# Performance work log

Hardware: AMD Instinct MI355X
Metric: run time of the kernel (lower is better)

Reference implementation:

```python
import jax, jax.numpy as jnp
import numpy as np

# dims / hyperparams (mirror init_kwargs)
B, N, C, K = 256, 16000, 32, 64          # batch, samples, cochlear channels, gammatone taps
FS, FMIN, FMAX, BWF = 16000, 100.0, 8000.0, 1.0
WINDOW, STRIDE = 256, 128                # inner hair cell framing -> T = 124
ANS, HID, OUT = 10, 50, 10               # auditory-nerve fanout, bushy/ic hidden, AC out
BETA, THR = 0.95, 1.0                    # snn.Leaky(beta=0.95), threshold 1.0, subtract reset
AN_LO, AN_HI, AN_THR = 0.5, 1.5, 0.5     # an_range scales + AN firing threshold

# Heaviside spike with ATan surrogate gradient (snntorch default style)
@jax.custom_vjp
def spike(u):
    return (u > 0).astype(u.dtype)

def _spike_fwd(u):
    return spike(u), u

def _spike_bwd(u, g):
    return (g / (1.0 + (jnp.pi * u) ** 2),)

spike.defvjp(_spike_fwd, _spike_bwd)

def _gammatone_bank():
    # ERB-spaced 4th-order gammatone impulse responses, unit L2 norm. [C, K]
    def hz2erb(f):
        return 21.4 * np.log10(1.0 + 0.00437 * f)
    def erb2hz(e):
        return (10.0 ** (e / 21.4) - 1.0) / 0.00437
    cfs = erb2hz(np.linspace(hz2erb(FMIN), hz2erb(FMAX), C))
    b = BWF * 1.019 * 24.7 * (4.37 * cfs / 1000.0 + 1.0)
    t = np.arange(K) / FS
    ker = (t[None, :] ** 3) * np.exp(-2 * np.pi * b[:, None] * t[None, :]) \
          * np.cos(2 * np.pi * cfs[:, None] * t[None, :])
    ker = ker / (np.linalg.norm(ker, axis=1, keepdims=True) + 1e-12)
    return jnp.asarray(ker, jnp.float32)

def setup_inputs() -> dict:
    key = jax.random.key(0)
    k1, k2, k3, k4 = jax.random.split(key, 4)
    audio = jax.random.normal(k1, (B, N), dtype=jnp.float32)
    W_bushy = jax.random.normal(k2, (HID, C * ANS), dtype=jnp.float32) / np.sqrt(C * ANS)
    W_ic = jax.random.normal(k3, (HID, HID), dtype=jnp.float32) / np.sqrt(HID)
    W_ac = jax.random.normal(k4, (OUT, HID), dtype=jnp.float32) / np.sqrt(HID)
    return {"audio": audio, "gt_kernels": _gammatone_bank(),
            "W_bushy": W_bushy, "W_ic": W_ic, "W_ac": W_ac}

def reference(audio, gt_kernels, W_bushy, W_ic, W_ac):
    # Cochlear: gammatone filterbank, [B,1,N] conv [C,1,K] SAME -> [B,C,N]
    y = jax.lax.conv_general_dilated(audio[:, None, :], gt_kernels[:, None, :],
                                     window_strides=(1,), padding="SAME")
    # InnerHairCell: half-wave rectify + moving-average framing -> [B,C,T]
    y = jnp.maximum(y, 0.0)
    env = jax.lax.reduce_window(y, 0.0, jax.lax.add,
                                (1, 1, WINDOW), (1, 1, STRIDE), "VALID") / WINDOW
    frames = jnp.transpose(env, (2, 0, 1))  # [T,B,C]
    scales = jnp.linspace(AN_LO, AN_HI, ANS, dtype=jnp.float32)

    def lif(mem, cur):
        mem = BETA * mem + cur
        spk = spike(mem - THR)
        return spk, mem - THR * spk  # subtract reset

    def step(carry, x_t):  # x_t [B,C]
        mem_b, mem_ic, mem_ac = carry
        # AuditoryNerve: ans scaled copies per channel, threshold fire -> [B, C*ANS]
        spk_an = spike(x_t[:, :, None] * scales - AN_THR).reshape(x_t.shape[0], -1)
        spk_b, mem_b = lif(mem_b, spk_an @ W_bushy.T)     # Bushy
        spk_ic, mem_ic = lif(mem_ic, spk_b @ W_ic.T)      # InferiorColliculus
        spk_ac, mem_ac = lif(mem_ac, spk_ic @ W_ac.T)     # AudioCortex
        return (mem_b, mem_ic, mem_ac), (spk_ac, mem_ac)

    bsz = audio.shape[0]
    init = (jnp.zeros((bsz, HID), audio.dtype),
            jnp.zeros((bsz, HID), audio.dtype),
            jnp.zeros((bsz, OUT), audio.dtype))
    _, (spk_rec, mem_rec) = jax.lax.scan(step, init, frames)
    # stack along dim=1 as in torch code -> [B,T,OUT]
    return jnp.transpose(spk_rec, (1, 0, 2)), jnp.transpose(mem_rec, (1, 0, 2))
```

## Files before the change

### kernel.cpp

```cpp
#include <hip/hip_runtime.h>

#define B_   256
#define N_   16000
#define C_   32
#define K_   64
#define T_   124
#define NJ   125
#define HID_ 50
#define OUT_ 10
#define TB_  1024
#define CURS 52

typedef unsigned int u32;
typedef float v2f __attribute__((ext_vector_type(2)));
struct __align__(16) f2x2 { v2f lo, hi; };

__device__ __forceinline__ float fadd(float a, float b) { return __fadd_rn(a, b); }
__device__ __forceinline__ float fmul(float a, float b) { return __fmul_rn(a, b); }
__device__ __forceinline__ float fsub(float a, float b) { return __fsub_rn(a, b); }

__device__ __forceinline__ void PKFMA(v2f& y, v2f a, const f2x2& T, int k) {
    switch (k) {
    case 0:  asm("v_pk_fma_f32 %0, %1, %2, %0 op_sel:[0,0,0] op_sel_hi:[1,0,1]"
                 : "+v"(y) : "v"(a), "s"(T.lo)); break;
    case 1:  asm("v_pk_fma_f32 %0, %1, %2, %0 op_sel:[0,1,0] op_sel_hi:[1,1,1]"
                 : "+v"(y) : "v"(a), "s"(T.lo)); break;
    case 2:  asm("v_pk_fma_f32 %0, %1, %2, %0 op_sel:[0,0,0] op_sel_hi:[1,0,1]"
                 : "+v"(y) : "v"(a), "s"(T.hi)); break;
    default: asm("v_pk_fma_f32 %0, %1, %2, %0 op_sel:[0,1,0] op_sel_hi:[1,1,1]"
                 : "+v"(y) : "v"(a), "s"(T.hi)); break;
    }
}

__global__ __launch_bounds__(256, 4) void convA(const float* __restrict__ audio,
                                                const float* __restrict__ gt,
                                                float* __restrict__ Sg) {
    __shared__ __align__(16) float abI[1280];
    __shared__ __align__(16) float ybuf[4][4][272];

    const int b = blockIdx.x, g = blockIdx.y;
    const int tid = threadIdx.x, w = tid >> 6, lane = tid & 63;
    const float* arow = audio + (size_t)b * N_;

    const int origin = (g << 10) - 32;
    for (int idx = tid; idx < 1280; idx += 256) {
        int P = idx / 640, j = idx - P * 640;
        int ii = j >> 1, h = j & 1;
        int gi = origin + (P << 9) + (h << 8) + ii;
        float v = (gi >= 0 && gi < N_) ? arow[gi] : 0.0f;
        abI[P * 640 + (j ^ (((j >> 5) & 1) << 2))] = v;
    }
    __syncthreads();

    for (int G = 0; G < 2; ++G) {
        const int rowbase = __builtin_amdgcn_readfirstlane(((w << 3) + (G << 2)) << 6);
        const float* kg = gt + rowbase;

        v2f Y[2][4][4];
#pragma unroll
        for (int P = 0; P < 2; ++P)
#pragma unroll
            for (int ch = 0; ch < 4; ++ch)
#pragma unroll
                for (int d = 0; d < 4; ++d) { Y[P][ch][d].x = 0.0f; Y[P][ch][d].y = 0.0f; }

        {
            f2x2 Tc[4];
#pragma unroll
            for (int ch = 0; ch < 4; ++ch)
                Tc[ch] = *(const f2x2*)(kg + (ch << 6));
            const int u = lane;
            const int p1 = (u << 3) ^ (((u >> 2) & 1) << 2);
#pragma unroll
            for (int P = 0; P < 2; ++P) {
                const float* abP = abI + P * 640;
                const f2x2 A0 = *(const f2x2*)(abP + p1);
                const f2x2 A1 = *(const f2x2*)(abP + (p1 ^ 4));
#pragma unroll
                for (int e = 0; e < 4; ++e) {
                    const v2f a = (e == 0) ? A0.lo : (e == 1) ? A0.hi
                                : (e == 2) ? A1.lo : A1.hi;
#pragma unroll
                    for (int ch = 0; ch < 4; ++ch)
#pragma unroll
                        for (int d = 0; d < 4; ++d) {
                            const int kb = e - 1 - d;
                            if (kb >= 0) PKFMA(Y[P][ch][d], a, Tc[ch], kb);
                        }
                }
            }
        }

#pragma unroll 1
        for (int q = 1; q < 16; ++q) {
            f2x2 Tm[4], Tc[4];
#pragma unroll
            for (int ch = 0; ch < 4; ++ch) {
                Tm[ch] = *(const f2x2*)(kg + (ch << 6) + ((q - 1) << 2));
                Tc[ch] = *(const f2x2*)(kg + (ch << 6) + (q << 2));
            }
            const int u = lane + q;
            const int p1 = (u << 3) ^ (((u >> 2) & 1) << 2);
#pragma unroll
            for (int P = 0; P < 2; ++P) {
                const float* abP = abI + P * 640;
                const f2x2 A0 = *(const f2x2*)(abP + p1);
                const f2x2 A1 = *(const f2x2*)(abP + (p1 ^ 4));
#pragma unroll
                for (int e = 0; e < 4; ++e) {
                    const v2f a = (e == 0) ? A0.lo : (e == 1) ? A0.hi
                                : (e == 2) ? A1.lo : A1.hi;
#pragma unroll
                    for (int ch = 0; ch < 4; ++ch)
#pragma unroll
                        for (int d = 0; d < 4; ++d) {
                            const int ts = e - 1 - d;
                            if (ts >= 0) PKFMA(Y[P][ch][d], a, Tc[ch], ts);
                            else         PKFMA(Y[P][ch][d], a, Tm[ch], 4 + ts);
                        }
                }
            }
        }

        {
            f2x2 Tm[4];
#pragma unroll
            for (int ch = 0; ch < 4; ++ch)
                Tm[ch] = *(const f2x2*)(kg + (ch << 6) + 60);
            const int u = lane + 16;
            const int p1 = (u << 3) ^ (((u >> 2) & 1) << 2);
#pragma unroll
            for (int P = 0; P < 2; ++P) {
                const float* abP = abI + P * 640;
                const f2x2 A0 = *(const f2x2*)(abP + p1);
                const f2x2 A1 = *(const f2x2*)(abP + (p1 ^ 4));
#pragma unroll
                for (int e = 0; e < 4; ++e) {
                    const v2f a = (e == 0) ? A0.lo : (e == 1) ? A0.hi
                                : (e == 2) ? A1.lo : A1.hi;
#pragma unroll
                    for (int ch = 0; ch < 4; ++ch)
#pragma unroll
                        for (int d = 0; d < 4; ++d) {
                            const int ts = e - 1 - d;
                            if (ts < 0) PKFMA(Y[P][ch][d], a, Tm[ch], 4 + ts);
                        }
                }
            }
        }

#pragma unroll
        for (int pp = 0; pp < 4; ++pp) {
            const int P = pp >> 1, h = pp & 1;
#pragma unroll
            for (int ch = 0; ch < 4; ++ch) {
                float4 z;
                z.x = fmaxf(h ? Y[P][ch][0].y : Y[P][ch][0].x, 0.0f);
                z.y = fmaxf(h ? Y[P][ch][1].y : Y[P][ch][1].x, 0.0f);
                z.z = fmaxf(h ? Y[P][ch][2].y : Y[P][ch][2].x, 0.0f);
                z.w = fmaxf(h ? Y[P][ch][3].y : Y[P][ch][3].x, 0.0f);
                *(float4*)(&ybuf[w][ch][((lane >> 5) * 136) + ((lane & 31) << 2)]) = z;
            }
            {
                const int ch2 = lane >> 4, blk = (lane >> 3) & 1, j = lane & 7;
                const float* yb = &ybuf[w][ch2][blk * 136 + j];
                float r = yb[0];
#pragma unroll
                for (int m = 1; m < 16; ++m) r = fadd(r, yb[m << 3]);
                float v = fadd(r, __shfl_xor(r, 1));
                v = fadd(v, __shfl_xor(v, 2));
                v = fadd(v, __shfl_xor(v, 4));
                const int jg = (g << 3) + (pp << 1) + blk;
                const int c = (w << 3) + (G << 2) + ch2;
                if (j == 0 && jg < NJ) Sg[((size_t)b * C_ + c) * NJ + jg] = v;
            }
        }
    }
}

__global__ __launch_bounds__(TB_, 1) void snnB(const float* __restrict__ Sg,
                                               const float* __restrict__ Wb,
                                               const float* __restrict__ Wic,
                                               const float* __restrict__ Wac,
                                               float* __restrict__ out) {
    __shared__ float sWb[HID_ * 321];
    __shared__ __align__(16) float sWic[HID_ * 52];
    __shared__ __align__(16) float sWac[OUT_ * 52];
    __shared__ u32   mask[128 * 10];
    __shared__ __align__(16) float cur[T_ * CURS];
    __shared__ __align__(16) float icur[T_ * CURS];
    __shared__ float acur[T_ * 12];

    const int b = blockIdx.x, tid = threadIdx.x;

    for (int i = tid; i < HID_ * 320; i += TB_) {
        int r = i / 320;
        sWb[r * 321 + (i - r * 320)] = Wb[i];
    }
    for (int i = tid; i < HID_ * HID_; i += TB_) {
        int r = i / 50;
        sWic[r * 52 + (i - r * 50)] = Wic[i];
    }
    for (int i = tid; i < OUT_ * HID_; i += TB_) {
        int r = i / 50;
        sWac[r * 52 + (i - r * 50)] = Wac[i];
    }

    const float* Sb = Sg + (size_t)b * C_ * NJ;
    for (int idx = tid; idx < 1280; idx += TB_) {
        if (idx >= T_ * 10) { mask[idx] = 0; continue; }
        int t = idx / 10, wd = idx - t * 10;
        u32 m = 0;
        int c_prev = -1;
        float env = 0.0f;
        for (int k = 0; k < 32; ++k) {
            int i = wd * 32 + k;
            int c = i / 10, s = i - c * 10;
            if (c != c_prev) {
                env = fmul(fadd(Sb[c * NJ + t], Sb[c * NJ + t + 1]), 0.00390625f);
                c_prev = c;
            }
            float sf = (s == 9) ? 1.5f : (float)(0.5 + (double)s * (1.0 / 9.0));
            if (fsub(fmul(env, sf), 0.5f) > 0.0f) m |= (1u << k);
        }
        mask[idx] = m;
    }
    __syncthreads();

    if (tid < 16 * HID_) {
        const int t0 = tid / 50, h = tid - t0 * 50;
        const float* wr = sWb + h * 321;
        const u32* mrow = mask + t0 * 10;
        float a0 = 0.0f, a1 = 0.0f, a2 = 0.0f, a3 = 0.0f;
        float a4 = 0.0f, a5 = 0.0f, a6 = 0.0f, a7 = 0.0f;
#pragma unroll 1
        for (int wi = 0; wi < 10; ++wi) {
            const u32 w0 = mrow[wi], w1 = mrow[160 + wi];
            const u32 w2 = mrow[320 + wi], w3 = mrow[480 + wi];
            const u32 w4 = mrow[640 + wi], w5 = mrow[800 + wi];
            const u32 w6 = mrow[960 + wi], w7 = mrow[1120 + wi];
#pragma unroll
            for (int b2 = 0; b2 < 32; ++b2) {
                const float wv = wr[(wi << 5) + b2];
                const int iw = __float_as_int(wv);
                a0 = fadd(a0, __int_as_float(iw & __builtin_amdgcn_sbfe((int)w0, b2, 1)));
                a1 = fadd(a1, __int_as_float(iw & __builtin_amdgcn_sbfe((int)w1, b2, 1)));
                a2 = fadd(a2, __int_as_float(iw & __builtin_amdgcn_sbfe((int)w2, b2, 1)));
                a3 = fadd(a3, __int_as_float(iw & __builtin_amdgcn_sbfe((int)w3, b2, 1)));
                a4 = fadd(a4, __int_as_float(iw & __builtin_amdgcn_sbfe((int)w4, b2, 1)));
                a5 = fadd(a5, __int_as_float(iw & __builtin_amdgcn_sbfe((int)w5, b2, 1)));
                a6 = fadd(a6, __int_as_float(iw & __builtin_amdgcn_sbfe((int)w6, b2, 1)));
                a7 = fadd(a7, __int_as_float(iw & __builtin_amdgcn_sbfe((int)w7, b2, 1)));
            }
        }
        cur[(t0      ) * CURS + h] = a0;
        cur[(t0 + 16 ) * CURS + h] = a1;
        cur[(t0 + 32 ) * CURS + h] = a2;
        cur[(t0 + 48 ) * CURS + h] = a3;
        cur[(t0 + 64 ) * CURS + h] = a4;
        cur[(t0 + 80 ) * CURS + h] = a5;
        cur[(t0 + 96 ) * CURS + h] = a6;
        if (t0 + 112 < T_) cur[(t0 + 112) * CURS + h] = a7;
    }
    __syncthreads();

    if (tid < HID_) {
        float mem = 0.0f;
        for (int t0 = 0; t0 < 120; t0 += 8) {
            float c0[8];
#pragma unroll
            for (int k = 0; k < 8; ++k) c0[k] = cur[(t0 + k) * CURS + tid];
#pragma unroll
            for (int k = 0; k < 8; ++k) {
                float m = fadd(fmul(0.95f, mem), c0[k]);
                float sp = (fsub(m, 1.0f) > 0.0f) ? 1.0f : 0.0f;
                mem = fsub(m, sp);
                cur[(t0 + k) * CURS + tid] = sp;
            }
        }
        for (int t = 120; t < T_; ++t) {
            float m = fadd(fmul(0.95f, mem), cur[t * CURS + tid]);
            float sp = (fsub(m, 1.0f) > 0.0f) ? 1.0f : 0.0f;
            mem = fsub(m, sp);
            cur[t * CURS + tid] = sp;
        }
    }
    __syncthreads();

    for (int idx = tid; idx < T_ * 25; idx += TB_) {
        int t = idx / 25, hp = idx - t * 25;
        const float* w0 = sWic + hp * 52;
        const float* w1 = sWic + (hp + 25) * 52;
        const float* sb = cur + t * CURS;
        float acc0 = 0.0f, acc1 = 0.0f;
#pragma unroll
        for (int g4 = 0; g4 < 12; ++g4) {
            const float4 s4 = *(const float4*)(sb + (g4 << 2));
            const float4 wa = *(const float4*)(w0 + (g4 << 2));
            const float4 wb = *(const float4*)(w1 + (g4 << 2));
            acc0 = fmaf(s4.x, wa.x, acc0);  acc1 = fmaf(s4.x, wb.x, acc1);
            acc0 = fmaf(s4.y, wa.y, acc0);  acc1 = fmaf(s4.y, wb.y, acc1);
            acc0 = fmaf(s4.z, wa.z, acc0);  acc1 = fmaf(s4.z, wb.z, acc1);
            acc0 = fmaf(s4.w, wa.w, acc0);  acc1 = fmaf(s4.w, wb.w, acc1);
        }
        acc0 = fmaf(sb[48], w0[48], acc0);  acc1 = fmaf(sb[48], w1[48], acc1);
        acc0 = fmaf(sb[49], w0[49], acc0);  acc1 = fmaf(sb[49], w1[49], acc1);
        icur[t * CURS + hp] = acc0;
        icur[t * CURS + hp + 25] = acc1;
    }
    __syncthreads();

    if (tid < HID_) {
        float mem = 0.0f;
        for (int t0 = 0; t0 < 120; t0 += 8) {
            float c0[8];
#pragma unroll
            for (int k = 0; k < 8; ++k) c0[k] = icur[(t0 + k) * CURS + tid];
#pragma unroll
            for (int k = 0; k < 8; ++k) {
                float m = fadd(fmul(0.95f, mem), c0[k]);
                float sp = (fsub(m, 1.0f) > 0.0f) ? 1.0f : 0.0f;
                mem = fsub(m, sp);
                icur[(t0 + k) * CURS + tid] = sp;
            }
        }
        for (int t = 120; t < T_; ++t) {
            float m = fadd(fmul(0.95f, mem), icur[t * CURS + tid]);
            float sp = (fsub(m, 1.0f) > 0.0f) ? 1.0f : 0.0f;
            mem = fsub(m, sp);
            icur[t * CURS + tid] = sp;
        }
    }
    __syncthreads();

    for (int idx = tid; idx < T_ * 5; idx += TB_) {
        int t = idx / 5, op = idx - t * 5;
        const float* w0 = sWac + op * 52;
        const float* w1 = sWac + (op + 5) * 52;
        const float* sb = icur + t * CURS;
        float acc0 = 0.0f, acc1 = 0.0f;
#pragma unroll
        for (int g4 = 0; g4 < 12; ++g4) {
            const float4 s4 = *(const float4*)(sb + (g4 << 2));
            const float4 wa = *(const float4*)(w0 + (g4 << 2));
            const float4 wb = *(const float4*)(w1 + (g4 << 2));
            acc0 = fmaf(s4.x, wa.x, acc0);  acc1 = fmaf(s4.x, wb.x, acc1);
            acc0 = fmaf(s4.y, wa.y, acc0);  acc1 = fmaf(s4.y, wb.y, acc1);
            acc0 = fmaf(s4.z, wa.z, acc0);  acc1 = fmaf(s4.z, wb.z, acc1);
            acc0 = fmaf(s4.w, wa.w, acc0);  acc1 = fmaf(s4.w, wb.w, acc1);
        }
        acc0 = fmaf(sb[48], w0[48], acc0);  acc1 = fmaf(sb[48], w1[48], acc1);
        acc0 = fmaf(sb[49], w0[49], acc0);  acc1 = fmaf(sb[49], w1[49], acc1);
        acur[t * 12 + op] = acc0;
        acur[t * 12 + op + 5] = acc1;
    }
    __syncthreads();

    if (tid < OUT_) {
        float mem = 0.0f;
        for (int t0 = 0; t0 < 120; t0 += 8) {
            float c0[8];
#pragma unroll
            for (int k = 0; k < 8; ++k) c0[k] = acur[(t0 + k) * 12 + tid];
#pragma unroll
            for (int k = 0; k < 8; ++k) {
                float m = fadd(fmul(0.95f, mem), c0[k]);
                float sp = (fsub(m, 1.0f) > 0.0f) ? 1.0f : 0.0f;
                float mo = fsub(m, sp);
                mem = mo;
                size_t base = ((size_t)b * T_ + (t0 + k)) * OUT_ + tid;
                out[base] = sp;
                out[(size_t)(B_ * T_ * OUT_) + base] = mo;
            }
        }
        for (int t = 120; t < T_; ++t) {
            float m = fadd(fmul(0.95f, mem), acur[t * 12 + tid]);
            float sp = (fsub(m, 1.0f) > 0.0f) ? 1.0f : 0.0f;
            float mo = fsub(m, sp);
            mem = mo;
            size_t base = ((size_t)b * T_ + t) * OUT_ + tid;
            out[base] = sp;
            out[(size_t)(B_ * T_ * OUT_) + base] = mo;
        }
    }
}

extern "C" void kernel_launch(void* const* d_in, const int* in_sizes, int n_in,
                              void* d_out, int out_size, void* d_ws, size_t ws_size,
                              hipStream_t stream) {
    (void)in_sizes; (void)n_in; (void)out_size; (void)ws_size;
    const float* audio = (const float*)d_in[0];
    const float* gt    = (const float*)d_in[1];
    const float* Wb    = (const float*)d_in[2];
    const float* Wic   = (const float*)d_in[3];
    const float* Wac   = (const float*)d_in[4];

    float* Sg = (float*)d_ws;

    convA<<<dim3(B_, 16), dim3(256), 0, stream>>>(audio, gt, Sg);
    snnB<<<dim3(B_), dim3(TB_), 0, stream>>>(Sg, Wb, Wic, Wac, (float*)d_out);
}
```

Before: 309.1 us.

## Split conv accumulators per half-block to raise occupancy; pack SNN adds

The conv kernel's loop is reordered so the P (audio half) loop is outermost with a single 4x4 accumulator set instead of 2x4x4, and launch bounds move from 4 to 6 waves per SIMD. The aim is to lower register pressure and raise occupancy. The cost is that the kernel taps are reloaded once per P. Separately, the bushy-current accumulation packs pairs of accumulators into v2f vectors so the compiler can emit packed f32 adds.

New measurement: 308.4 us. Within noise of the previous version (-0.2%).

```diff
diff --git a/kernel.cpp b/kernel.cpp
--- a/kernel.cpp
+++ b/kernel.cpp
@@ -32,7 +32,7 @@
     }
 }
 
-__global__ __launch_bounds__(256, 4) void convA(const float* __restrict__ audio,
+__global__ __launch_bounds__(256, 6) void convA(const float* __restrict__ audio,
                                                 const float* __restrict__ gt,
                                                 float* __restrict__ Sg) {
     __shared__ __align__(16) float abI[1280];
@@ -52,28 +52,27 @@
     }
     __syncthreads();
 
-    for (int G = 0; G < 2; ++G) {
-        const int rowbase = __builtin_amdgcn_readfirstlane(((w << 3) + (G << 2)) << 6);
-        const float* kg = gt + rowbase;
-
-        v2f Y[2][4][4];
-#pragma unroll
-        for (int P = 0; P < 2; ++P)
+#pragma unroll 1
+    for (int P = 0; P < 2; ++P) {
+        const float* abP = abI + P * 640;
+#pragma unroll 1
+        for (int G = 0; G < 2; ++G) {
+            const int rowbase = __builtin_amdgcn_readfirstlane(((w << 3) + (G << 2)) << 6);
+            const float* kg = gt + rowbase;
+
+            v2f Y[4][4];
 #pragma unroll
             for (int ch = 0; ch < 4; ++ch)
 #pragma unroll
-                for (int d = 0; d < 4; ++d) { Y[P][ch][d].x = 0.0f; Y[P][ch][d].y = 0.0f; }
-
-        {
-            f2x2 Tc[4];
-#pragma unroll
-            for (int ch = 0; ch < 4; ++ch)
-                Tc[ch] = *(const f2x2*)(kg + (ch << 6));
-            const int u = lane;
-            const int p1 = (u << 3) ^ (((u >> 2) & 1) << 2);
-#pragma unroll
-            for (int P = 0; P < 2; ++P) {
-                const float* abP = abI + P * 640;
+                for (int d = 0; d < 4; ++d) { Y[ch][d].x = 0.0f; Y[ch][d].y = 0.0f; }
+
+            {
+                f2x2 Tc[4];
+#pragma unroll
+                for (int ch = 0; ch < 4; ++ch)
+                    Tc[ch] = *(const f2x2*)(kg + (ch << 6));
+                const int u = lane;
+                const int p1 = (u << 3) ^ (((u >> 2) & 1) << 2);
                 const f2x2 A0 = *(const f2x2*)(abP + p1);
                 const f2x2 A1 = *(const f2x2*)(abP + (p1 ^ 4));
 #pragma unroll
@@ -85,25 +84,21 @@
 #pragma unroll
                         for (int d = 0; d < 4; ++d) {
                             const int kb = e - 1 - d;
-                            if (kb >= 0) PKFMA(Y[P][ch][d], a, Tc[ch], kb);
+                            if (kb >= 0) PKFMA(Y[ch][d], a, Tc[ch], kb);
                         }
                 }
             }
-        }
 
 #pragma unroll 1
-        for (int q = 1; q < 16; ++q) {
-            f2x2 Tm[4], Tc[4];
-#pragma unroll
-            for (int ch = 0; ch < 4; ++ch) {
-                Tm[ch] = *(const f2x2*)(kg + (ch << 6) + ((q - 1) << 2));
-                Tc[ch] = *(const f2x2*)(kg + (ch << 6) + (q << 2));
-            }
-            const int u = lane + q;
-            const int p1 = (u << 3) ^ (((u >> 2) & 1) << 2);
-#pragma unroll
-            for (int P = 0; P < 2; ++P) {
-                const float* abP = abI + P * 640;
+            for (int q = 1; q < 16; ++q) {
+                f2x2 Tm[4], Tc[4];
+#pragma unroll
+                for (int ch = 0; ch < 4; ++ch) {
+                    Tm[ch] = *(const f2x2*)(kg + (ch << 6) + ((q - 1) << 2));
+                    Tc[ch] = *(const f2x2*)(kg + (ch << 6) + (q << 2));
+                }
+                const int u = lane + q;
+                const int p1 = (u << 3) ^ (((u >> 2) & 1) << 2);
                 const f2x2 A0 = *(const f2x2*)(abP + p1);
                 const f2x2 A1 = *(const f2x2*)(abP + (p1 ^ 4));
 #pragma unroll
@@ -115,23 +110,19 @@
 #pragma unroll
                         for (int d = 0; d < 4; ++d) {
                             const int ts = e - 1 - d;
-                            if (ts >= 0) PKFMA(Y[P][ch][d], a, Tc[ch], ts);
-                            else         PKFMA(Y[P][ch][d], a, Tm[ch], 4 + ts);
+                            if (ts >= 0) PKFMA(Y[ch][d], a, Tc[ch], ts);
+                            else         PKFMA(Y[ch][d], a, Tm[ch], 4 + ts);
                         }
                 }
             }
-        }
-
-        {
-            f2x2 Tm[4];
-#pragma unroll
-            for (int ch = 0; ch < 4; ++ch)
-                Tm[ch] = *(const f2x2*)(kg + (ch << 6) + 60);
-            const int u = lane + 16;
-            const int p1 = (u << 3) ^ (((u >> 2) & 1) << 2);
-#pragma unroll
-            for (int P = 0; P < 2; ++P) {
-                const float* abP = abI + P * 640;
+
+            {
+                f2x2 Tm[4];
+#pragma unroll
+                for (int ch = 0; ch < 4; ++ch)
+                    Tm[ch] = *(const f2x2*)(kg + (ch << 6) + 60);
+                const int u = lane + 16;
+                const int p1 = (u << 3) ^ (((u >> 2) & 1) << 2);
                 const f2x2 A0 = *(const f2x2*)(abP + p1);
                 const f2x2 A1 = *(const f2x2*)(abP + (p1 ^ 4));
 #pragma unroll
@@ -143,36 +134,36 @@
 #pragma unroll
                         for (int d = 0; d < 4; ++d) {
                             const int ts = e - 1 - d;
-                            if (ts < 0) PKFMA(Y[P][ch][d], a, Tm[ch], 4 + ts);
+                            if (ts < 0) PKFMA(Y[ch][d], a, Tm[ch], 4 + ts);
                         }
                 }
             }
-        }
-
-#pragma unroll
-        for (int pp = 0; pp < 4; ++pp) {
-            const int P = pp >> 1, h = pp & 1;
-#pragma unroll
-            for (int ch = 0; ch < 4; ++ch) {
-                float4 z;
-                z.x = fmaxf(h ? Y[P][ch][0].y : Y[P][ch][0].x, 0.0f);
-                z.y = fmaxf(h ? Y[P][ch][1].y : Y[P][ch][1].x, 0.0f);
-                z.z = fmaxf(h ? Y[P][ch][2].y : Y[P][ch][2].x, 0.0f);
-                z.w = fmaxf(h ? Y[P][ch][3].y : Y[P][ch][3].x, 0.0f);
-                *(float4*)(&ybuf[w][ch][((lane >> 5) * 136) + ((lane & 31) << 2)]) = z;
-            }
-            {
-                const int ch2 = lane >> 4, blk = (lane >> 3) & 1, j = lane & 7;
-                const float* yb = &ybuf[w][ch2][blk * 136 + j];
-                float r = yb[0];
-#pragma unroll
-                for (int m = 1; m < 16; ++m) r = fadd(r, yb[m << 3]);
-                float v = fadd(r, __shfl_xor(r, 1));
-                v = fadd(v, __shfl_xor(v, 2));
-                v = fadd(v, __shfl_xor(v, 4));
-                const int jg = (g << 3) + (pp << 1) + blk;
-                const int c = (w << 3) + (G << 2) + ch2;
-                if (j == 0 && jg < NJ) Sg[((size_t)b * C_ + c) * NJ + jg] = v;
+
+#pragma unroll
+            for (int h = 0; h < 2; ++h) {
+                const int pp = (P << 1) + h;
+#pragma unroll
+                for (int ch = 0; ch < 4; ++ch) {
+                    float4 z;
+                    z.x = fmaxf(h ? Y[ch][0].y : Y[ch][0].x, 0.0f);
+                    z.y = fmaxf(h ? Y[ch][1].y : Y[ch][1].x, 0.0f);
+                    z.z = fmaxf(h ? Y[ch][2].y : Y[ch][2].x, 0.0f);
+                    z.w = fmaxf(h ? Y[ch][3].y : Y[ch][3].x, 0.0f);
+                    *(float4*)(&ybuf[w][ch][((lane >> 5) * 136) + ((lane & 31) << 2)]) = z;
+                }
+                {
+                    const int ch2 = lane >> 4, blk = (lane >> 3) & 1, j = lane & 7;
+                    const float* yb = &ybuf[w][ch2][blk * 136 + j];
+                    float r = yb[0];
+#pragma unroll
+                    for (int m = 1; m < 16; ++m) r = fadd(r, yb[m << 3]);
+                    float v = fadd(r, __shfl_xor(r, 1));
+                    v = fadd(v, __shfl_xor(v, 2));
+                    v = fadd(v, __shfl_xor(v, 4));
+                    const int jg = (g << 3) + (pp << 1) + blk;
+                    const int c = (w << 3) + (G << 2) + ch2;
+                    if (j == 0 && jg < NJ) Sg[((size_t)b * C_ + c) * NJ + jg] = v;
+                }
             }
         }
     }
@@ -231,8 +222,8 @@
         const int t0 = tid / 50, h = tid - t0 * 50;
         const float* wr = sWb + h * 321;
         const u32* mrow = mask + t0 * 10;
-        float a0 = 0.0f, a1 = 0.0f, a2 = 0.0f, a3 = 0.0f;
-        float a4 = 0.0f, a5 = 0.0f, a6 = 0.0f, a7 = 0.0f;
+        v2f A0v = {0.0f, 0.0f}, A1v = {0.0f, 0.0f};
+        v2f A2v = {0.0f, 0.0f}, A3v = {0.0f, 0.0f};
 #pragma unroll 1
         for (int wi = 0; wi < 10; ++wi) {
             const u32 w0 = mrow[wi], w1 = mrow[160 + wi];
@@ -243,24 +234,29 @@
             for (int b2 = 0; b2 < 32; ++b2) {
                 const float wv = wr[(wi << 5) + b2];
                 const int iw = __float_as_int(wv);
-                a0 = fadd(a0, __int_as_float(iw & __builtin_amdgcn_sbfe((int)w0, b2, 1)));
-                a1 = fadd(a1, __int_as_float(iw & __builtin_amdgcn_sbfe((int)w1, b2, 1)));
-                a2 = fadd(a2, __int_as_float(iw & __builtin_amdgcn_sbfe((int)w2, b2, 1)));
-                a3 = fadd(a3, __int_as_float(iw & __builtin_amdgcn_sbfe((int)w3, b2, 1)));
-                a4 = fadd(a4, __int_as_float(iw & __builtin_amdgcn_sbfe((int)w4, b2, 1)));
-                a5 = fadd(a5, __int_as_float(iw & __builtin_amdgcn_sbfe((int)w5, b2, 1)));
-                a6 = fadd(a6, __int_as_float(iw & __builtin_amdgcn_sbfe((int)w6, b2, 1)));
-                a7 = fadd(a7, __int_as_float(iw & __builtin_amdgcn_sbfe((int)w7, b2, 1)));
-            }
-        }
-        cur[(t0      ) * CURS + h] = a0;
-        cur[(t0 + 16 ) * CURS + h] = a1;
-        cur[(t0 + 32 ) * CURS + h] = a2;
-        cur[(t0 + 48 ) * CURS + h] = a3;
-        cur[(t0 + 64 ) * CURS + h] = a4;
-        cur[(t0 + 80 ) * CURS + h] = a5;
-        cur[(t0 + 96 ) * CURS + h] = a6;
-        if (t0 + 112 < T_) cur[(t0 + 112) * CURS + h] = a7;
+                v2f p0, p1, p2, p3;
+                p0.x = __int_as_float(iw & __builtin_amdgcn_sbfe((int)w0, b2, 1));
+                p0.y = __int_as_float(iw & __builtin_amdgcn_sbfe((int)w1, b2, 1));
+                p1.x = __int_as_float(iw & __builtin_amdgcn_sbfe((int)w2, b2, 1));
+                p1.y = __int_as_float(iw & __builtin_amdgcn_sbfe((int)w3, b2, 1));
+                p2.x = __int_as_float(iw & __builtin_amdgcn_sbfe((int)w4, b2, 1));
+                p2.y = __int_as_float(iw & __builtin_amdgcn_sbfe((int)w5, b2, 1));
+                p3.x = __int_as_float(iw & __builtin_amdgcn_sbfe((int)w6, b2, 1));
+                p3.y = __int_as_float(iw & __builtin_amdgcn_sbfe((int)w7, b2, 1));
+                A0v = A0v + p0;
+                A1v = A1v + p1;
+                A2v = A2v + p2;
+                A3v = A3v + p3;
+            }
+        }
+        cur[(t0      ) * CURS + h] = A0v.x;
+        cur[(t0 + 16 ) * CURS + h] = A0v.y;
+        cur[(t0 + 32 ) * CURS + h] = A1v.x;
+        cur[(t0 + 48 ) * CURS + h] = A1v.y;
+        cur[(t0 + 64 ) * CURS + h] = A2v.x;
+        cur[(t0 + 80 ) * CURS + h] = A2v.y;
+        cur[(t0 + 96 ) * CURS + h] = A3v.x;
+        if (t0 + 112 < T_) cur[(t0 + 112) * CURS + h] = A3v.y;
     }
     __syncthreads();
 
```

## Retile SNN bushy/IC/AC matmuls as 2x4 register tiles with packed adds

Applied to the files above, without the earlier changes.

The bushy-layer masked accumulation now has each thread compute two hidden units across four timesteps, with paired v2f adds, instead of one hidden unit across eight timesteps. Weight-row stride goes to 324 and the weights are loaded with float4 copies. The IC and AC projections are retiled the same way (4 timesteps x 2 outputs per thread, 775 or 155 threads) so each weight vector load is reused across timesteps. The aim is fewer LDS loads per FLOP and more ILP in the SNN kernel, at the cost of more registers per thread and changed LDS bank patterns.

Measured after the change: 290.7 us, median of 2. 6.0% less time.

```diff
diff --git a/kernel.cpp b/kernel.cpp
--- a/kernel.cpp
+++ b/kernel.cpp
@@ -10,6 +10,7 @@
 #define OUT_ 10
 #define TB_  1024
 #define CURS 52
+#define WBS  324
 
 typedef unsigned int u32;
 typedef float v2f __attribute__((ext_vector_type(2)));
@@ -183,7 +184,7 @@
                                                const float* __restrict__ Wic,
                                                const float* __restrict__ Wac,
                                                float* __restrict__ out) {
-    __shared__ float sWb[HID_ * 321];
+    __shared__ __align__(16) float sWb[HID_ * WBS];
     __shared__ __align__(16) float sWic[HID_ * 52];
     __shared__ __align__(16) float sWac[OUT_ * 52];
     __shared__ u32   mask[128 * 10];
@@ -193,9 +194,10 @@
 
     const int b = blockIdx.x, tid = threadIdx.x;
 
-    for (int i = tid; i < HID_ * 320; i += TB_) {
-        int r = i / 320;
-        sWb[r * 321 + (i - r * 320)] = Wb[i];
+    for (int i4 = tid; i4 < 4000; i4 += TB_) {
+        const int i = i4 << 2;
+        const int r = i / 320, col = i - r * 320;
+        *(float4*)(&sWb[r * WBS + col]) = *(const float4*)(Wb + i);
     }
     for (int i = tid; i < HID_ * HID_; i += TB_) {
         int r = i / 50;
@@ -227,40 +229,41 @@
     }
     __syncthreads();
 
-    if (tid < 16 * HID_) {
-        const int t0 = tid / 50, h = tid - t0 * 50;
-        const float* wr = sWb + h * 321;
+    if (tid < 31 * 25) {
+        const int t0 = tid / 25, hp = tid - t0 * 25;
+        const float* wr0 = sWb + hp * WBS;
+        const float* wr1 = sWb + (hp + 25) * WBS;
         const u32* mrow = mask + t0 * 10;
-        float a0 = 0.0f, a1 = 0.0f, a2 = 0.0f, a3 = 0.0f;
-        float a4 = 0.0f, a5 = 0.0f, a6 = 0.0f, a7 = 0.0f;
+        v2f a0 = {0.0f, 0.0f}, a1 = {0.0f, 0.0f};
+        v2f a2 = {0.0f, 0.0f}, a3 = {0.0f, 0.0f};
 #pragma unroll 1
         for (int wi = 0; wi < 10; ++wi) {
-            const u32 w0 = mrow[wi], w1 = mrow[160 + wi];
-            const u32 w2 = mrow[320 + wi], w3 = mrow[480 + wi];
-            const u32 w4 = mrow[640 + wi], w5 = mrow[800 + wi];
-            const u32 w6 = mrow[960 + wi], w7 = mrow[1120 + wi];
+            const u32 w0 = mrow[wi],       w1 = mrow[310 + wi];
+            const u32 w2 = mrow[620 + wi], w3 = mrow[930 + wi];
 #pragma unroll
             for (int b2 = 0; b2 < 32; ++b2) {
-                const float wv = wr[(wi << 5) + b2];
-                const int iw = __float_as_int(wv);
-                a0 = fadd(a0, __int_as_float(iw & __builtin_amdgcn_sbfe((int)w0, b2, 1)));
-                a1 = fadd(a1, __int_as_float(iw & __builtin_amdgcn_sbfe((int)w1, b2, 1)));
-                a2 = fadd(a2, __int_as_float(iw & __builtin_amdgcn_sbfe((int)w2, b2, 1)));
-                a3 = fadd(a3, __int_as_float(iw & __builtin_amdgcn_sbfe((int)w3, b2, 1)));
-                a4 = fadd(a4, __int_as_float(iw & __builtin_amdgcn_sbfe((int)w4, b2, 1)));
-                a5 = fadd(a5, __int_as_float(iw & __builtin_amdgcn_sbfe((int)w5, b2, 1)));
-                a6 = fadd(a6, __int_as_float(iw & __builtin_amdgcn_sbfe((int)w6, b2, 1)));
-                a7 = fadd(a7, __int_as_float(iw & __builtin_amdgcn_sbfe((int)w7, b2, 1)));
-            }
-        }
-        cur[(t0      ) * CURS + h] = a0;
-        cur[(t0 + 16 ) * CURS + h] = a1;
-        cur[(t0 + 32 ) * CURS + h] = a2;
-        cur[(t0 + 48 ) * CURS + h] = a3;
-        cur[(t0 + 64 ) * CURS + h] = a4;
-        cur[(t0 + 80 ) * CURS + h] = a5;
-        cur[(t0 + 96 ) * CURS + h] = a6;
-        if (t0 + 112 < T_) cur[(t0 + 112) * CURS + h] = a7;
+                const int i = (wi << 5) + b2;
+                const int iw0 = __float_as_int(wr0[i]);
+                const int iw1 = __float_as_int(wr1[i]);
+                const int s0 = __builtin_amdgcn_sbfe((int)w0, b2, 1);
+                const int s1 = __builtin_amdgcn_sbfe((int)w1, b2, 1);
+                const int s2 = __builtin_amdgcn_sbfe((int)w2, b2, 1);
+                const int s3 = __builtin_amdgcn_sbfe((int)w3, b2, 1);
+                v2f p0, p1, p2, p3;
+                p0.x = __int_as_float(iw0 & s0);  p0.y = __int_as_float(iw1 & s0);
+                p1.x = __int_as_float(iw0 & s1);  p1.y = __int_as_float(iw1 & s1);
+                p2.x = __int_as_float(iw0 & s2);  p2.y = __int_as_float(iw1 & s2);
+                p3.x = __int_as_float(iw0 & s3);  p3.y = __int_as_float(iw1 & s3);
+                a0 = a0 + p0;
+                a1 = a1 + p1;
+                a2 = a2 + p2;
+                a3 = a3 + p3;
+            }
+        }
+        cur[(t0     ) * CURS + hp] = a0.x;  cur[(t0     ) * CURS + hp + 25] = a0.y;
+        cur[(t0 + 31) * CURS + hp] = a1.x;  cur[(t0 + 31) * CURS + hp + 25] = a1.y;
+        cur[(t0 + 62) * CURS + hp] = a2.x;  cur[(t0 + 62) * CURS + hp + 25] = a2.y;
+        cur[(t0 + 93) * CURS + hp] = a3.x;  cur[(t0 + 93) * CURS + hp + 25] = a3.y;
     }
     __syncthreads();
 
@@ -287,26 +290,53 @@
     }
     __syncthreads();
 
-    for (int idx = tid; idx < T_ * 25; idx += TB_) {
-        int t = idx / 25, hp = idx - t * 25;
+    if (tid < 31 * 25) {
+        const int t0 = tid / 25, hp = tid - t0 * 25;
         const float* w0 = sWic + hp * 52;
         const float* w1 = sWic + (hp + 25) * 52;
-        const float* sb = cur + t * CURS;
-        float acc0 = 0.0f, acc1 = 0.0f;
+        const float* sb0 = cur + (t0     ) * CURS;
+        const float* sb1 = cur + (t0 + 31) * CURS;
+        const float* sb2 = cur + (t0 + 62) * CURS;
+        const float* sb3 = cur + (t0 + 93) * CURS;
+        float A00 = 0.0f, A01 = 0.0f, A10 = 0.0f, A11 = 0.0f;
+        float A20 = 0.0f, A21 = 0.0f, A30 = 0.0f, A31 = 0.0f;
 #pragma unroll
         for (int g4 = 0; g4 < 12; ++g4) {
-            const float4 s4 = *(const float4*)(sb + (g4 << 2));
             const float4 wa = *(const float4*)(w0 + (g4 << 2));
             const float4 wb = *(const float4*)(w1 + (g4 << 2));
-            acc0 = fmaf(s4.x, wa.x, acc0);  acc1 = fmaf(s4.x, wb.x, acc1);
-            acc0 = fmaf(s4.y, wa.y, acc0);  acc1 = fmaf(s4.y, wb.y, acc1);
-            acc0 = fmaf(s4.z, wa.z, acc0);  acc1 = fmaf(s4.z, wb.z, acc1);
-            acc0 = fmaf(s4.w, wa.w, acc0);  acc1 = fmaf(s4.w, wb.w, acc1);
-        }
-        acc0 = fmaf(sb[48], w0[48], acc0);  acc1 = fmaf(sb[48], w1[48], acc1);
-        acc0 = fmaf(sb[49], w0[49], acc0);  acc1 = fmaf(sb[49], w1[49], acc1);
-        icur[t * CURS + hp] = acc0;
-        icur[t * CURS + hp + 25] = acc1;
+            const float4 s0 = *(const float4*)(sb0 + (g4 << 2));
+            const float4 s1 = *(const float4*)(sb1 + (g4 << 2));
+            const float4 s2 = *(const float4*)(sb2 + (g4 << 2));
+            const float4 s3 = *(const float4*)(sb3 + (g4 << 2));
+            A00 = fmaf(s0.x, wa.x, A00); A00 = fmaf(s0.y, wa.y, A00);
+            A00 = fmaf(s0.z, wa.z, A00); A00 = fmaf(s0.w, wa.w, A00);
+            A01 = fmaf(s0.x, wb.x, A01); A01 = fmaf(s0.y, wb.y, A01);
+            A01 = fmaf(s0.z, wb.z, A01); A01 = fmaf(s0.w, wb.w, A01);
+            A10 = fmaf(s1.x, wa.x, A10); A10 = fmaf(s1.y, wa.y, A10);
+            A10 = fmaf(s1.z, wa.z, A10); A10 = fmaf(s1.w, wa.w, A10);
+            A11 = fmaf(s1.x, wb.x, A11); A11 = fmaf(s1.y, wb.y, A11);
+            A11 = fmaf(s1.z, wb.z, A11); A11 = fmaf(s1.w, wb.w, A11);
+            A20 = fmaf(s2.x, wa.x, A20); A20 = fmaf(s2.y, wa.y, A20);
+            A20 = fmaf(s2.z, wa.z, A20); A20 = fmaf(s2.w, wa.w, A20);
+            A21 = fmaf(s2.x, wb.x, A21); A21 = fmaf(s2.y, wb.y, A21);
+            A21 = fmaf(s2.z, wb.z, A21); A21 = fmaf(s2.w, wb.w, A21);
+            A30 = fmaf(s3.x, wa.x, A30); A30 = fmaf(s3.y, wa.y, A30);
+            A30 = fmaf(s3.z, wa.z, A30); A30 = fmaf(s3.w, wa.w, A30);
+            A31 = fmaf(s3.x, wb.x, A31); A31 = fmaf(s3.y, wb.y, A31);
+            A31 = fmaf(s3.z, wb.z, A31); A31 = fmaf(s3.w, wb.w, A31);
+        }
+        A00 = fmaf(sb0[48], w0[48], A00); A00 = fmaf(sb0[49], w0[49], A00);
+        A01 = fmaf(sb0[48], w1[48], A01); A01 = fmaf(sb0[49], w1[49], A01);
+        A10 = fmaf(sb1[48], w0[48], A10); A10 = fmaf(sb1[49], w0[49], A10);
+        A11 = fmaf(sb1[48], w1[48], A11); A11 = fmaf(sb1[49], w1[49], A11);
+        A20 = fmaf(sb2[48], w0[48], A20); A20 = fmaf(sb2[49], w0[49], A20);
+        A21 = fmaf(sb2[48], w1[48], A21); A21 = fmaf(sb2[49], w1[49], A21);
+        A30 = fmaf(sb3[48], w0[48], A30); A30 = fmaf(sb3[49], w0[49], A30);
+        A31 = fmaf(sb3[48], w1[48], A31); A31 = fmaf(sb3[49], w1[49], A31);
+        icur[(t0     ) * CURS + hp] = A00;  icur[(t0     ) * CURS + hp + 25] = A01;
+        icur[(t0 + 31) * CURS + hp] = A10;  icur[(t0 + 31) * CURS + hp + 25] = A11;
+        icur[(t0 + 62) * CURS + hp] = A20;  icur[(t0 + 62) * CURS + hp + 25] = A21;
+        icur[(t0 + 93) * CURS + hp] = A30;  icur[(t0 + 93) * CURS + hp + 25] = A31;
     }
     __syncthreads();
 
@@ -333,26 +363,53 @@
     }
     __syncthreads();
 
-    for (int idx = tid; idx < T_ * 5; idx += TB_) {
-        int t = idx / 5, op = idx - t * 5;
+    if (tid < 31 * 5) {
+        const int t0 = tid / 5, op = tid - t0 * 5;
         const float* w0 = sWac + op * 52;
         const float* w1 = sWac + (op + 5) * 52;
-        const float* sb = icur + t * CURS;
-        float acc0 = 0.0f, acc1 = 0.0f;
+        const float* sb0 = icur + (t0     ) * CURS;
+        const float* sb1 = icur + (t0 + 31) * CURS;
+        const float* sb2 = icur + (t0 + 62) * CURS;
+        const float* sb3 = icur + (t0 + 93) * CURS;
+        float A00 = 0.0f, A01 = 0.0f, A10 = 0.0f, A11 = 0.0f;
+        float A20 = 0.0f, A21 = 0.0f, A30 = 0.0f, A31 = 0.0f;
 #pragma unroll
         for (int g4 = 0; g4 < 12; ++g4) {
-            const float4 s4 = *(const float4*)(sb + (g4 << 2));
             const float4 wa = *(const float4*)(w0 + (g4 << 2));
             const float4 wb = *(const float4*)(w1 + (g4 << 2));
-            acc0 = fmaf(s4.x, wa.x, acc0);  acc1 = fmaf(s4.x, wb.x, acc1);
-            acc0 = fmaf(s4.y, wa.y, acc0);  acc1 = fmaf(s4.y, wb.y, acc1);
-            acc0 = fmaf(s4.z, wa.z, acc0);  acc1 = fmaf(s4.z, wb.z, acc1);
-            acc0 = fmaf(s4.w, wa.w, acc0);  acc1 = fmaf(s4.w, wb.w, acc1);
-        }
-        acc0 = fmaf(sb[48], w0[48], acc0);  acc1 = fmaf(sb[48], w1[48], acc1);
-        acc0 = fmaf(sb[49], w0[49], acc0);  acc1 = fmaf(sb[49], w1[49], acc1);
-        acur[t * 12 + op] = acc0;
-        acur[t * 12 + op + 5] = acc1;
+            const float4 s0 = *(const float4*)(sb0 + (g4 << 2));
+            const float4 s1 = *(const float4*)(sb1 + (g4 << 2));
+            const float4 s2 = *(const float4*)(sb2 + (g4 << 2));
+            const float4 s3 = *(const float4*)(sb3 + (g4 << 2));
+            A00 = fmaf(s0.x, wa.x, A00); A00 = fmaf(s0.y, wa.y, A00);
+            A00 = fmaf(s0.z, wa.z, A00); A00 = fmaf(s0.w, wa.w, A00);
+            A01 = fmaf(s0.x, wb.x, A01); A01 = fmaf(s0.y, wb.y, A01);
+            A01 = fmaf(s0.z, wb.z, A01); A01 = fmaf(s0.w, wb.w, A01);
+            A10 = fmaf(s1.x, wa.x, A10); A10 = fmaf(s1.y, wa.y, A10);
+            A10 = fmaf(s1.z, wa.z, A10); A10 = fmaf(s1.w, wa.w, A10);
+            A11 = fmaf(s1.x, wb.x, A11); A11 = fmaf(s1.y, wb.y, A11);
+            A11 = fmaf(s1.z, wb.z, A11); A11 = fmaf(s1.w, wb.w, A11);
+            A20 = fmaf(s2.x, wa.x, A20); A20 = fmaf(s2.y, wa.y, A20);
+            A20 = fmaf(s2.z, wa.z, A20); A20 = fmaf(s2.w, wa.w, A20);
+            A21 = fmaf(s2.x, wb.x, A21); A21 = fmaf(s2.y, wb.y, A21);
+            A21 = fmaf(s2.z, wb.z, A21); A21 = fmaf(s2.w, wb.w, A21);
+            A30 = fmaf(s3.x, wa.x, A30); A30 = fmaf(s3.y, wa.y, A30);
+            A30 = fmaf(s3.z, wa.z, A30); A30 = fmaf(s3.w, wa.w, A30);
+            A31 = fmaf(s3.x, wb.x, A31); A31 = fmaf(s3.y, wb.y, A31);
+            A31 = fmaf(s3.z, wb.z, A31); A31 = fmaf(s3.w, wb.w, A31);
+        }
+        A00 = fmaf(sb0[48], w0[48], A00); A00 = fmaf(sb0[49], w0[49], A00);
+        A01 = fmaf(sb0[48], w1[48], A01); A01 = fmaf(sb0[49], w1[49], A01);
+        A10 = fmaf(sb1[48], w0[48], A10); A10 = fmaf(sb1[49], w0[49], A10);
+        A11 = fmaf(sb1[48], w1[48], A11); A11 = fmaf(sb1[49], w1[49], A11);
+        A20 = fmaf(sb2[48], w0[48], A20); A20 = fmaf(sb2[49], w0[49], A20);
+        A21 = fmaf(sb2[48], w1[48], A21); A21 = fmaf(sb2[49], w1[49], A21);
+        A30 = fmaf(sb3[48], w0[48], A30); A30 = fmaf(sb3[49], w0[49], A30);
+        A31 = fmaf(sb3[48], w1[48], A31); A31 = fmaf(sb3[49], w1[49], A31);
+        acur[(t0     ) * 12 + op] = A00;  acur[(t0     ) * 12 + op + 5] = A01;
+        acur[(t0 + 31) * 12 + op] = A10;  acur[(t0 + 31) * 12 + op + 5] = A11;
+        acur[(t0 + 62) * 12 + op] = A20;  acur[(t0 + 62) * 12 + op + 5] = A21;
+        acur[(t0 + 93) * 12 + op] = A30;  acur[(t0 + 93) * 12 + op + 5] = A31;
     }
     __syncthreads();
 
```
